# Kernel optimization log

Measured on AMD Instinct MI355X. Metric: run time of the kernel, lower is better.

The kernel has to match this reference:

```python
import jax, jax.numpy as jnp
import numpy as np

B, Qn, Kn, QD, KVD, FFN, H = 8, 1024, 2048, 512, 256, 2048, 8


def _layer_norm(x, g, b, eps=1e-5):
    m = jnp.mean(x, axis=-1, keepdims=True)
    v = jnp.mean((x - m) ** 2, axis=-1, keepdims=True)
    return (x - m) * jax.lax.rsqrt(v + eps) * g + b


def _mha(q, k, v, key_padding_mask, num_heads):
    # q,k: [B,S,D], v: [B,K,Dv]; reshape to per-head, scale by sqrt(key head dim)
    b, qn, d = q.shape
    kn = k.shape[1]
    dh = d // num_heads
    q = q.reshape(b, qn, num_heads, dh)
    k = k.reshape(b, kn, num_heads, dh)
    v = v.reshape(b, kn, num_heads, -1)
    attn = jnp.einsum('bqhd,bkhd->bhqk', q, k) / jnp.asarray(np.sqrt(dh), q.dtype)
    attn = jnp.where(key_padding_mask[:, None, None, :], -jnp.inf, attn)
    attn = jax.nn.softmax(attn, axis=-1)
    out = jnp.einsum('bhqk,bkhd->bqhd', attn, v)  # [B,Q,H,dv]
    return out.reshape(b, qn, -1)


def setup_inputs() -> dict:
    key = jax.random.key(0)
    ks = jax.random.split(key, 32)
    s = 0.02
    inp = {
        'queries_data': jax.random.normal(ks[0], (B, Qn, QD), jnp.float32),
        'queries_mask': jnp.zeros((B, Qn), bool),
        'box_pos': jax.random.normal(ks[1], (B, Qn, 4 * KVD), jnp.float32),
        'center_pos': jax.random.normal(ks[2], (B, Qn, 2 * KVD), jnp.float32),
        'kv_data': jax.random.normal(ks[3], (B, Kn, KVD), jnp.float32),
        'kv_mask': jnp.zeros((B, Kn), bool),
        'kv_pos': jax.random.normal(ks[4], (B, Kn, KVD), jnp.float32),
        # params ([in,out] convention)
        'sa_qkv_w': jax.random.normal(ks[5], (QD, 3 * QD), jnp.float32) * s,
        'sa_qkv_b': jnp.zeros((3 * QD,), jnp.float32),
        'sa_pos_w': jax.random.normal(ks[6], (4 * KVD, 2 * QD), jnp.float32) * s,
        'sa_pos_b': jnp.zeros((2 * QD,), jnp.float32),
        'sa_ln_g': jnp.ones((QD,), jnp.float32),
        'sa_ln_b': jnp.zeros((QD,), jnp.float32),
        'ca_q_w': jax.random.normal(ks[7], (QD, QD), jnp.float32) * s,
        'ca_q_b': jnp.zeros((QD,), jnp.float32),
        'ca_kv_w': jax.random.normal(ks[8], (KVD, 2 * QD), jnp.float32) * s,
        'ca_kv_b': jnp.zeros((2 * QD,), jnp.float32),
        'ca_qpos_w': jax.random.normal(ks[9], (2 * KVD, QD), jnp.float32) * s,
        'ca_qpos_b': jnp.zeros((QD,), jnp.float32),
        'ca_kpos_w': jax.random.normal(ks[10], (KVD, QD), jnp.float32) * s,
        'ca_kpos_b': jnp.zeros((QD,), jnp.float32),
        'ca_ln_g': jnp.ones((QD,), jnp.float32),
        'ca_ln_b': jnp.zeros((QD,), jnp.float32),
        'ffn_w1': jax.random.normal(ks[11], (QD, FFN), jnp.float32) * s,
        'ffn_b1': jnp.zeros((FFN,), jnp.float32),
        'ffn_w2': jax.random.normal(ks[12], (FFN, QD), jnp.float32) * s,
        'ffn_b2': jnp.zeros((QD,), jnp.float32),
        'ffn_ln_g': jnp.ones((QD,), jnp.float32),
        'ffn_ln_b': jnp.zeros((QD,), jnp.float32),
    }
    return inp


def reference(queries_data, queries_mask, box_pos, center_pos, kv_data, kv_mask, kv_pos,
              sa_qkv_w, sa_qkv_b, sa_pos_w, sa_pos_b, sa_ln_g, sa_ln_b,
              ca_q_w, ca_q_b, ca_kv_w, ca_kv_b, ca_qpos_w, ca_qpos_b,
              ca_kpos_w, ca_kpos_b, ca_ln_g, ca_ln_b,
              ffn_w1, ffn_b1, ffn_w2, ffn_b2, ffn_ln_g, ffn_ln_b):
    # ---- self-attention (pos added to q,k) ----
    qkv = queries_data @ sa_qkv_w + sa_qkv_b
    q, k, v = jnp.split(qkv, 3, axis=-1)
    q_pos, k_pos = jnp.split(box_pos @ sa_pos_w + sa_pos_b, 2, axis=-1)
    sa_out = _mha(q + q_pos, k + k_pos, v, queries_mask, H)
    sa_out = _layer_norm(queries_data + sa_out, sa_ln_g, sa_ln_b)
    # ---- cross-attention (pos concatenated per head) ----
    q = sa_out @ ca_q_w + ca_q_b
    k, v = jnp.split(kv_data @ ca_kv_w + ca_kv_b, 2, axis=-1)
    q_pos = center_pos @ ca_qpos_w + ca_qpos_b
    k_pos = kv_pos @ ca_kpos_w + ca_kpos_b
    dh = QD // H
    q = jnp.concatenate([q.reshape(B, Qn, H, dh), q_pos.reshape(B, Qn, H, dh)], axis=-1).reshape(B, Qn, -1)
    k = jnp.concatenate([k.reshape(B, Kn, H, dh), k_pos.reshape(B, Kn, H, dh)], axis=-1).reshape(B, Kn, -1)
    ca_out = _mha(q, k, v, kv_mask, H)
    ca_out = _layer_norm(sa_out + ca_out, ca_ln_g, ca_ln_b)
    # ---- FFN ----
    f = jax.nn.relu(ca_out @ ffn_w1 + ffn_b1) @ ffn_w2 + ffn_b2
    return _layer_norm(ca_out + f, ffn_ln_g, ffn_ln_b)
```

## Files before the change

kernel.cpp:

```cpp
#include <hip/hip_runtime.h>

typedef __attribute__((ext_vector_type(4))) float f32x4;
typedef __attribute__((ext_vector_type(8))) short bf16x8;
typedef __attribute__((ext_vector_type(4))) unsigned int u32x4;

static __device__ __forceinline__ float bf2f(short s){
    unsigned int u = ((unsigned int)(unsigned short)s) << 16;
    return __builtin_bit_cast(float, u);
}
static __device__ __forceinline__ short f2bf(float f){
    unsigned int u = __builtin_bit_cast(unsigned int, f);
    unsigned int r = (u + 0x7fffu + ((u >> 16) & 1u)) >> 16;
    return (short)r;
}
static __device__ __forceinline__ void gload_lds16(const void* g, void* l){
    __builtin_amdgcn_global_load_lds((const __attribute__((address_space(1))) void*)g,
                                     (__attribute__((address_space(3))) void*)l, 16, 0, 0);
}
static __device__ __forceinline__ float exp2fast(float x){
    float r; asm("v_exp_f32 %0, %1" : "=v"(r) : "v"(x)); return r;
}
static __device__ __forceinline__ unsigned int packbf(float lo, float hi){
#if __has_builtin(__builtin_amdgcn_perm)
    return __builtin_amdgcn_perm(__builtin_bit_cast(unsigned int, hi),
                                 __builtin_bit_cast(unsigned int, lo), 0x07060302u);
#else
    return (__builtin_bit_cast(unsigned int, hi) & 0xffff0000u) |
           (__builtin_bit_cast(unsigned int, lo) >> 16);
#endif
}
static __device__ __forceinline__ void prio_hi(){
#if defined(__HIP_DEVICE_COMPILE__)
    __builtin_amdgcn_s_setprio(1);
#endif
}
static __device__ __forceinline__ void prio_lo(){
#if defined(__HIP_DEVICE_COMPILE__)
    __builtin_amdgcn_s_setprio(0);
#endif
}

static __device__ __forceinline__ void transcast_body(const float* __restrict__ w,
                                                      short* __restrict__ wT,
                                                      int K, int N, int bx, int by, int t){
    int n = bx * 256 + t;
    int k0 = by * 8;
    bf16x8 o;
#pragma unroll
    for (int j = 0; j < 8; j++) o[j] = f2bf(w[(long)(k0 + j) * N + n]);
    *(bf16x8*)(wT + (long)n * K + k0) = o;
}
__global__ __launch_bounds__(256) void prep_weights(
    const float* __restrict__ queries, const float* __restrict__ box,
    const float* __restrict__ ctr, const float* __restrict__ kvd, const float* __restrict__ kvp,
    const unsigned char* __restrict__ qmask, const unsigned char* __restrict__ kmask,
    const float* __restrict__ b_qkv, const float* __restrict__ b_pos,
    short* __restrict__ Xcat, short* __restrict__ ctr_bf,
    short* __restrict__ kvd_bf, short* __restrict__ kvp_bf,
    float* __restrict__ mb_sa, float* __restrict__ mb_ca, float* __restrict__ bcomb,
    const float* __restrict__ w_qkv, const float* __restrict__ w_pos,
    const float* __restrict__ w_caq, const float* __restrict__ w_cakv,
    const float* __restrict__ w_caqp, const float* __restrict__ w_cakp,
    const float* __restrict__ w_f1, const float* __restrict__ w_f2,
    short* __restrict__ wTm_qk, short* __restrict__ wTv,
    short* __restrict__ wT_caq, short* __restrict__ wT_cakv,
    short* __restrict__ wT_caqp, short* __restrict__ wT_cakp,
    short* __restrict__ wT_f1, short* __restrict__ wT_f2)
{
    int bb = blockIdx.x, t = threadIdx.x;
    if (bb < 12288){
        const float* src; short* dst; long i; long stride; int logRow; int colOff;
        if (bb < 2048){ src = queries; dst = Xcat; i = ((long)bb * 256 + t) * 8; logRow = 9;  stride = 1536; colOff = 0; }
        else if (bb < 6144){ src = box; dst = Xcat; i = ((long)(bb - 2048) * 256 + t) * 8; logRow = 10; stride = 1536; colOff = 512; }
        else if (bb < 8192){ src = ctr; dst = ctr_bf; i = ((long)(bb - 6144) * 256 + t) * 8; logRow = 0; stride = 0; colOff = 0; }
        else if (bb < 10240){ src = kvd; dst = kvd_bf; i = ((long)(bb - 8192) * 256 + t) * 8; logRow = 0; stride = 0; colOff = 0; }
        else { src = kvp; dst = kvp_bf; i = ((long)(bb - 10240) * 256 + t) * 8; logRow = 0; stride = 0; colOff = 0; }
        f32x4 a = *(const f32x4*)(src + i);
        f32x4 b = *(const f32x4*)(src + i + 4);
        bf16x8 o;
#pragma unroll
        for (int j = 0; j < 4; j++){ o[j] = f2bf(a[j]); o[4 + j] = f2bf(b[j]); }
        long oi = logRow ? ((i >> logRow) * stride + colOff + (i & ((1L << logRow) - 1))) : i;
        *(bf16x8*)(dst + oi) = o;
        return;
    }
    if (bb < 12320){ int i = (bb - 12288) * 256 + t; mb_sa[i] = qmask[i] ? -1e30f : 0.f; return; }
    if (bb < 12384){ int i = (bb - 12320) * 256 + t; mb_ca[i] = kmask[i] ? -1e30f : 0.f; return; }
    if (bb < 12388){ int i = (bb - 12384) * 256 + t; if (i < 1024) bcomb[i] = b_qkv[i] + b_pos[i]; return; }
    int wb = bb - 12388;
    if (wb < 768){
        int by = wb / 4, bx = wb % 4;
        int n = bx * 256 + t;
        int k0 = by * 8;
        bf16x8 o;
#pragma unroll
        for (int j = 0; j < 8; j++){
            int kk = k0 + j;
            float v = (kk < 512) ? w_qkv[(long)kk * 1536 + n] : w_pos[(long)(kk - 512) * 1024 + n];
            o[j] = f2bf(v);
        }
        *(bf16x8*)(wTm_qk + (long)n * 1536 + k0) = o;
    }
    else if (wb < 896){
        int lb = wb - 768;
        int by = lb / 2, bx = lb % 2;
        int n = bx * 256 + t;
        int k0 = by * 8;
        bf16x8 o;
#pragma unroll
        for (int j = 0; j < 8; j++) o[j] = f2bf(w_qkv[(long)(k0 + j) * 1536 + 1024 + n]);
        *(bf16x8*)(wTv + (long)n * 512 + k0) = o;
    }
    else if (wb < 1024){ int lb = wb - 896;  transcast_body(w_caq,  wT_caq,  512, 512,  lb % 2, lb / 2, t); }
    else if (wb < 1152){ int lb = wb - 1024; transcast_body(w_cakv, wT_cakv, 256, 1024, lb % 4, lb / 4, t); }
    else if (wb < 1280){ int lb = wb - 1152; transcast_body(w_caqp, wT_caqp, 512, 512,  lb % 2, lb / 2, t); }
    else if (wb < 1344){ int lb = wb - 1280; transcast_body(w_cakp, wT_cakp, 256, 512,  lb % 2, lb / 2, t); }
    else if (wb < 1856){ int lb = wb - 1344; transcast_body(w_f1,   wT_f1,   512, 2048, lb % 8, lb / 8, t); }
    else               { int lb = wb - 1856; transcast_body(w_f2,   wT_f2,   2048, 512, lb % 2, lb / 2, t); }
}

struct GD {
    const short* A; const short* Bt; const float* bias;
    short* Cbf; float* Cf; short* Vt;
    long lda;
    int N, K, flags, vtColBase, snShift, vtSN, blkStart, nbx, nblk;
};
struct GD6 { GD g[6]; int n; };

static __device__ void gemm_body(char* smem, const GD6& dd, int bb)
{
    constexpr int BN = 128, BLOCK = 256;
    constexpr int BUF = (128 + BN) * 32;
    constexpr int EST = BN + 4;
    float* lC = (float*)smem;
    int si = 0;
#pragma unroll
    for (int i = 1; i < 6; i++) if (i < dd.n && bb >= dd.g[i].blkStart) si = i;
    const short* A = dd.g[si].A;
    const short* Bt = dd.g[si].Bt;
    const float* bias = dd.g[si].bias;
    short* Cbf = dd.g[si].Cbf;
    float* Cf = dd.g[si].Cf;
    short* Vt = dd.g[si].Vt;
    long lda = dd.g[si].lda;
    int N = dd.g[si].N, K = dd.g[si].K, flags = dd.g[si].flags;
    int vtColBase = dd.g[si].vtColBase, snShift = dd.g[si].snShift, vtSN = dd.g[si].vtSN;
    int nbx = dd.g[si].nbx, nblk = dd.g[si].nblk;

    int t = threadIdx.x, w = t >> 6, l = t & 63;
    int cl = l & 15, g = l >> 4;
    int flat = bb - dd.g[si].blkStart;
    int q8 = nblk >> 3;
    int swz = (flat & 7) * q8 + (flat >> 3);
    long r0 = (long)(swz / nbx) * 128, c0 = (long)(swz % nbx) * BN;
    int wr = w >> 1, wc = w & 1;
    f32x4 acc[4][4];
#pragma unroll
    for (int mi = 0; mi < 4; mi++)
#pragma unroll
        for (int ni = 0; ni < 4; ni++) acc[mi][ni] = f32x4{0.f, 0.f, 0.f, 0.f};

    auto stage = [&](int d, int k0){
        char* lA = smem + (size_t)d * BUF * 2;
        char* lB = lA + 128 * 32 * 2;
#pragma unroll
        for (int i = 0; i < 2; i++){
            int s = i * BLOCK + t;
            int row = s >> 2, blk = s & 3;
            int sb = blk ^ (row & 3);
            gload_lds16(A + (r0 + row) * lda + k0 + sb * 8, lA + i * 4096 + w * 1024);
        }
#pragma unroll
        for (int i = 0; i < 2; i++){
            int s = i * BLOCK + t;
            int row = s >> 2, blk = s & 3;
            int sb = blk ^ (row & 3);
            gload_lds16(Bt + (c0 + row) * (long)K + k0 + sb * 8, lB + i * 4096 + w * 1024);
        }
    };

    stage(0, 0);
    __syncthreads();
    int NK = K / 32;
    for (int kt = 0; kt < NK; kt++){
        int cur = kt & 1;
        if (kt + 1 < NK) stage(cur ^ 1, (kt + 1) * 32);
        const short* lA = (const short*)(smem + (size_t)cur * BUF * 2);
        const short* lB = lA + 128 * 32;
        bf16x8 af[4], bfr[4];
#pragma unroll
        for (int mi = 0; mi < 4; mi++){
            int row = wr * 64 + mi * 16 + cl;
            af[mi] = *(const bf16x8*)(lA + row * 32 + (g ^ (row & 3)) * 8);
        }
#pragma unroll
        for (int ni = 0; ni < 4; ni++){
            int row = wc * 64 + ni * 16 + cl;
            bfr[ni] = *(const bf16x8*)(lB + row * 32 + (g ^ (row & 3)) * 8);
        }
        prio_hi();
#pragma unroll
        for (int mi = 0; mi < 4; mi++)
#pragma unroll
            for (int ni = 0; ni < 4; ni++)
                acc[mi][ni] = __builtin_amdgcn_mfma_f32_16x16x32_bf16(af[mi], bfr[ni], acc[mi][ni], 0, 0, 0);
        prio_lo();
        __syncthreads();
    }

    bool vtBlock = (flags & 4) && (c0 >= vtColBase);
#pragma unroll
    for (int mi = 0; mi < 4; mi++){
        __syncthreads();
#pragma unroll
        for (int ni = 0; ni < 4; ni++)
#pragma unroll
            for (int rr = 0; rr < 4; rr++)
                lC[(wr * 16 + g * 4 + rr) * EST + wc * 64 + ni * 16 + cl] = acc[mi][ni][rr];
        __syncthreads();
        if (vtBlock){
#pragma unroll
            for (int c2 = 0; c2 < 2; c2++){
                int task = t + BLOCK * c2;
                int col = task & (BN - 1);
                int wrg = (task >> 7) & 1;
                int ch = task >> 8;
                float bv = bias[c0 + col];
                long qg0 = r0 + wrg * 64 + mi * 16 + ch * 8;
                bf16x8 ob;
#pragma unroll
                for (int j = 0; j < 8; j++)
                    ob[j] = f2bf(lC[(wrg * 16 + ch * 8 + j) * EST + col] + bv);
                long dvg = c0 - vtColBase + col;
                long h = dvg >> 6, dvv = dvg & 63;
                long b = qg0 >> snShift;
                long loc = qg0 & ((1L << snShift) - 1);
                *(bf16x8*)(Vt + ((b * 8 + h) * 64 + dvv) * (long)vtSN + loc) = ob;
            }
        } else {
            constexpr int CPR = BN / 8;
#pragma unroll
            for (int c2 = 0; c2 < 32 * CPR / BLOCK; c2++){
                int chunk = t + BLOCK * c2;
                int row = chunk / CPR;
                int coloff = (chunk % CPR) * 8;
                long grow = r0 + (row >> 4) * 64 + mi * 16 + (row & 15);
                long gcol = c0 + coloff;
                f32x4 bv0 = *(const f32x4*)(bias + gcol);
                f32x4 bv1 = *(const f32x4*)(bias + gcol + 4);
                float v[8];
#pragma unroll
                for (int j = 0; j < 8; j++){
                    float x = lC[row * EST + coloff + j] + (j < 4 ? bv0[j] : bv1[j - 4]);
                    if (flags & 1) x = fmaxf(x, 0.f);
                    v[j] = x;
                }
                if (Cf){
                    *(f32x4*)(Cf + grow * N + gcol) = f32x4{v[0], v[1], v[2], v[3]};
                    *(f32x4*)(Cf + grow * N + gcol + 4) = f32x4{v[4], v[5], v[6], v[7]};
                } else {
                    bf16x8 ob;
#pragma unroll
                    for (int j = 0; j < 8; j++) ob[j] = f2bf(v[j]);
                    long idx;
                    if (flags & 2){
                        long part = gcol >> 9;
                        long cc = gcol & 511;
                        long b = grow >> 10, qn = grow & 1023;
                        long h = cc >> 6, d = cc & 63;
                        idx = ((part * 64 + b * 8 + h) * 1024 + qn) * 64 + d;
                    } else if (flags & 4){
                        idx = grow * (long)vtColBase + gcol;
                    } else {
                        idx = grow * N + gcol;
                    }
                    *(bf16x8*)(Cbf + idx) = ob;
                }
            }
        }
    }
}

__global__ __launch_bounds__(256, 4) void gemm_multi(GD6 dd){
    __shared__ __attribute__((aligned(16))) char smem[32768];
    gemm_body(smem, dd, blockIdx.x);
}

struct AttnArgs {
    const short *Q1, *Q2, *K1, *K2, *Vt;
    const float* mbias; short* out; float scale2;
};

template<int DH, int KN, bool CAT>
static __device__ void attn_body(char* smemraw, const AttnArgs& a, int bid)
{
    constexpr int KT = 64, DV = 64, Qn = 1024, H = 8;
    constexpr int NF = DH / 32;
    constexpr int BPR = DH / 8;
    constexpr int KITER = KT * BPR / 256;
    constexpr int NT = KN / KT;
    short (*lK)[KT * DH] = (short(*)[KT * DH])smemraw;
    short (*lV)[DV * KT] = (short(*)[DV * KT])(smemraw + 2 * KT * DH * 2);
    const short* Q1 = a.Q1; const short* Q2 = a.Q2;
    const short* K1 = a.K1; const short* K2 = a.K2;
    const short* Vt = a.Vt;
    float scale2 = a.scale2;
    int t = threadIdx.x, w = t >> 6, l = t & 63;
    int cl = l & 15, g = l >> 4;
    int bh = (bid & 7) * 8 + (bid >> 6);
    int qb = (bid >> 3) & 7;
    int b = bh >> 3, h = bh & 7;
    int q0 = qb * 128 + w * 32;

    bf16x8 qf[2][NF];
#pragma unroll
    for (int qq = 0; qq < 2; qq++)
#pragma unroll
        for (int f = 0; f < NF; f++){
            if constexpr (CAT){
                const short* src = (f < NF / 2) ? Q1 : Q2;
                qf[qq][f] = *(const bf16x8*)(src + ((long)b * Qn + q0 + qq * 16 + cl) * 512 + h * 64
                                             + (f & (NF / 2 - 1)) * 32 + 8 * g);
            } else {
                qf[qq][f] = *(const bf16x8*)(Q1 + ((long)bh * Qn + q0 + qq * 16 + cl) * DH + f * 32 + 8 * g);
            }
        }

    const short* kp[KITER];
    long kstep[KITER];
#pragma unroll
    for (int i = 0; i < KITER; i++){
        int s_ = i * 256 + t;
        int srow_ = s_ / BPR, blk = s_ % BPR;
        int s32 = srow_ & 31;
        int key = (srow_ & 32) + 8 * ((s32 >> 2) & 3) + 4 * (s32 >> 4) + (s32 & 3);
        int sb = blk ^ (srow_ & 7);
        if constexpr (CAT){
            if (sb < 8){ kp[i] = K1 + ((long)b * KN + key) * 512 + h * 64 + sb * 8; kstep[i] = (long)KT * 512; }
            else       { kp[i] = K2 + ((long)b * KN + key) * 512 + h * 64 + (sb - 8) * 8; kstep[i] = (long)KT * 512; }
        } else {
            kp[i] = K1 + ((long)bh * KN + key) * DH + sb * 8; kstep[i] = (long)KT * DH;
        }
    }
    const short* vp[2];
#pragma unroll
    for (int i = 0; i < 2; i++){
        int s_ = i * 256 + t;
        int srow_ = s_ >> 3, blk = s_ & 7;
        int sb = blk ^ (srow_ & 7);
        vp[i] = Vt + ((long)bh * DV + srow_) * KN + sb * 8;
    }

    auto stage = [&](int d){
#pragma unroll
        for (int i = 0; i < KITER; i++){
            gload_lds16(kp[i], (char*)(&lK[d][0]) + i * 4096 + w * 1024);
            kp[i] += kstep[i];
        }
#pragma unroll
        for (int i = 0; i < 2; i++){
            gload_lds16(vp[i], (char*)(&lV[d][0]) + i * 4096 + w * 1024);
            vp[i] += KT;
        }
    };

    f32x4 st[2][4];
    auto do_qk = [&](int d){
        prio_hi();
#pragma unroll
        for (int o = 0; o < 4; o++){
            int srow_ = o * 16 + cl;
            bf16x8 kf[NF];
#pragma unroll
            for (int f = 0; f < NF; f++){
                int sb = (4 * f + g) ^ (srow_ & 7);
                kf[f] = *(const bf16x8*)(&lK[d][0] + srow_ * DH + sb * 8);
            }
#pragma unroll
            for (int qq = 0; qq < 2; qq++){
                f32x4 acc = f32x4{0.f, 0.f, 0.f, 0.f};
#pragma unroll
                for (int f = 0; f < NF; f++)
                    acc = __builtin_amdgcn_mfma_f32_16x16x32_bf16(kf[f], qf[qq][f], acc, 0, 0, 0);
                st[qq][o] = acc;
            }
        }
        prio_lo();
    };

    const float* mrow = a.mbias + (long)b * KN;
    bf16x8 vones;
    {
        u32x4 ou; ou[0] = ou[1] = ou[2] = ou[3] = 0x3F803F80u;
        vones = __builtin_bit_cast(bf16x8, ou);
    }
    f32x4 lacc[2];
    f32x4 oacc[2][4];
#pragma unroll
    for (int qq = 0; qq < 2; qq++){
        lacc[qq] = f32x4{0.f, 0.f, 0.f, 0.f};
#pragma unroll
        for (int d = 0; d < 4; d++) oacc[qq][d] = f32x4{0.f, 0.f, 0.f, 0.f};
    }

    f32x4 mb[4];
#pragma unroll
    for (int o = 0; o < 4; o++)
        mb[o] = *(const f32x4*)(mrow + (o >> 1) * 32 + 8 * g + 4 * (o & 1));

    stage(0);
    __syncthreads();
    do_qk(0);

    for (int tt = 0; tt < NT; tt++){
        int cur = tt & 1;
        if (tt + 1 < NT) stage(cur ^ 1);

        bf16x8 pa[2][2];
#pragma unroll
        for (int qq = 0; qq < 2; qq++){
#pragma unroll
            for (int kb = 0; kb < 2; kb++){
                float pA[4], pB[4];
#pragma unroll
                for (int rr = 0; rr < 4; rr++){
                    pA[rr] = exp2fast(fmaf(st[qq][2 * kb][rr], scale2, mb[2 * kb][rr]));
                    pB[rr] = exp2fast(fmaf(st[qq][2 * kb + 1][rr], scale2, mb[2 * kb + 1][rr]));
                }
                u32x4 pk;
                pk[0] = packbf(pA[0], pA[1]);
                pk[1] = packbf(pA[2], pA[3]);
                pk[2] = packbf(pB[0], pB[1]);
                pk[3] = packbf(pB[2], pB[3]);
                pa[qq][kb] = __builtin_bit_cast(bf16x8, pk);
            }
        }
        if (tt + 1 < NT){
#pragma unroll
            for (int o = 0; o < 4; o++)
                mb[o] = *(const f32x4*)(mrow + (tt + 1) * KT + (o >> 1) * 32 + 8 * g + 4 * (o & 1));
        }
        prio_hi();
#pragma unroll
        for (int qq = 0; qq < 2; qq++){
            lacc[qq] = __builtin_amdgcn_mfma_f32_16x16x32_bf16(pa[qq][0], vones, lacc[qq], 0, 0, 0);
            lacc[qq] = __builtin_amdgcn_mfma_f32_16x16x32_bf16(pa[qq][1], vones, lacc[qq], 0, 0, 0);
        }
#pragma unroll
        for (int dvc = 0; dvc < 4; dvc++){
            int vrow = dvc * 16 + cl;
            bf16x8 vf[2];
#pragma unroll
            for (int kb = 0; kb < 2; kb++){
                int sb = (4 * kb + g) ^ (vrow & 7);
                vf[kb] = *(const bf16x8*)(&lV[cur][0] + vrow * KT + sb * 8);
            }
#pragma unroll
            for (int qq = 0; qq < 2; qq++){
                f32x4 o = oacc[qq][dvc];
                o = __builtin_amdgcn_mfma_f32_16x16x32_bf16(pa[qq][0], vf[0], o, 0, 0, 0);
                o = __builtin_amdgcn_mfma_f32_16x16x32_bf16(pa[qq][1], vf[1], o, 0, 0, 0);
                oacc[qq][dvc] = o;
            }
        }
        prio_lo();
        __syncthreads();
        if (tt + 1 < NT) do_qk(cur ^ 1);
    }

#pragma unroll
    for (int qq = 0; qq < 2; qq++){
        float linv[4];
#pragma unroll
        for (int rr = 0; rr < 4; rr++) linv[rr] = 1.f / lacc[qq][rr];
#pragma unroll
        for (int dvc = 0; dvc < 4; dvc++)
#pragma unroll
            for (int rr = 0; rr < 4; rr++){
                int q = q0 + qq * 16 + 4 * g + rr;
                a.out[(((long)b * Qn + q) * H + h) * DV + dvc * 16 + cl] = f2bf(oacc[qq][dvc][rr] * linv[rr]);
            }
    }
}

__global__ __launch_bounds__(256, 2) void attn_ca(AttnArgs a){
    __shared__ __attribute__((aligned(16))) char smem[2 * 64 * 128 * 2 + 2 * 64 * 64 * 2];
    attn_body<128, 2048, true>(smem, a, blockIdx.x);
}

__global__ __launch_bounds__(256, 2) void attn_sa_gemm(AttnArgs a, GD6 dd, int nAttn){
    __shared__ __attribute__((aligned(16))) char smem[32768];
    if ((int)blockIdx.x < nAttn) attn_body<64, 1024, false>(smem, a, blockIdx.x);
    else gemm_body(smem, dd, blockIdx.x - nAttn);
}

__global__ __launch_bounds__(256) void ln_fuse(const float* __restrict__ a, const short* __restrict__ b,
                                               const float* __restrict__ g, const float* __restrict__ be,
                                               float* __restrict__ outf, short* __restrict__ outb){
    int w = threadIdx.x >> 6, l = threadIdx.x & 63;
    long row = (long)blockIdx.x * 4 + w;
    long base = row * 512 + l * 8;
    f32x4 a0 = *(const f32x4*)(a + base);
    f32x4 a1 = *(const f32x4*)(a + base + 4);
    bf16x8 bb = *(const bf16x8*)(b + base);
    float x[8]; float s = 0.f, s2 = 0.f;
#pragma unroll
    for (int j = 0; j < 4; j++){ x[j] = a0[j] + bf2f(bb[j]); x[4 + j] = a1[j] + bf2f(bb[4 + j]); }
#pragma unroll
    for (int j = 0; j < 8; j++){ s += x[j]; s2 += x[j] * x[j]; }
#pragma unroll
    for (int o = 1; o < 64; o <<= 1){ s += __shfl_xor(s, o); s2 += __shfl_xor(s2, o); }
    float mean = s * (1.f / 512.f);
    float rstd = rsqrtf(s2 * (1.f / 512.f) - mean * mean + 1e-5f);
    int c = l * 8;
    f32x4 y0, y1; bf16x8 ob;
#pragma unroll
    for (int j = 0; j < 4; j++){
        float y = (x[j] - mean) * rstd * g[c + j] + be[c + j];
        y0[j] = y; ob[j] = f2bf(y);
    }
#pragma unroll
    for (int j = 0; j < 4; j++){
        float y = (x[4 + j] - mean) * rstd * g[c + 4 + j] + be[c + 4 + j];
        y1[j] = y; ob[4 + j] = f2bf(y);
    }
    *(f32x4*)(outf + base) = y0;
    *(f32x4*)(outf + base + 4) = y1;
    if (outb) *(bf16x8*)(outb + base) = ob;
}

extern "C" void kernel_launch(void* const* d_in, const int* in_sizes, int n_in,
                              void* d_out, int out_size, void* d_ws, size_t ws_size,
                              hipStream_t stream)
{
    (void)in_sizes; (void)n_in; (void)out_size; (void)ws_size;
    const int Qn = 1024, Kn = 2048;
    const long MQ = 8L * Qn;
    const long MK = 8L * Kn;

    const float* queries = (const float*)d_in[0];
    const unsigned char* qmask = (const unsigned char*)d_in[1];
    const float* box  = (const float*)d_in[2];
    const float* ctr  = (const float*)d_in[3];
    const float* kvd  = (const float*)d_in[4];
    const unsigned char* kmask = (const unsigned char*)d_in[5];
    const float* kvp  = (const float*)d_in[6];
    const float* w_qkv = (const float*)d_in[7];  const float* b_qkv = (const float*)d_in[8];
    const float* w_pos = (const float*)d_in[9];  const float* b_pos = (const float*)d_in[10];
    const float* g_sa  = (const float*)d_in[11]; const float* be_sa = (const float*)d_in[12];
    const float* w_caq = (const float*)d_in[13]; const float* b_caq = (const float*)d_in[14];
    const float* w_cakv = (const float*)d_in[15]; const float* b_cakv = (const float*)d_in[16];
    const float* w_caqp = (const float*)d_in[17]; const float* b_caqp = (const float*)d_in[18];
    const float* w_cakp = (const float*)d_in[19]; const float* b_cakp = (const float*)d_in[20];
    const float* g_ca  = (const float*)d_in[21]; const float* be_ca = (const float*)d_in[22];
    const float* w_f1  = (const float*)d_in[23]; const float* b_f1 = (const float*)d_in[24];
    const float* w_f2  = (const float*)d_in[25]; const float* b_f2 = (const float*)d_in[26];
    const float* g_f   = (const float*)d_in[27]; const float* be_f = (const float*)d_in[28];

    char* ws = (char*)d_ws;
    size_t off = 0;
    auto alloc = [&](size_t bytes) -> char* {
        char* p = ws + off;
        off += (bytes + 255) & ~(size_t)255;
        return p;
    };
    short* wTm_qk  = (short*)alloc(1024L * 1536 * 2);
    short* wTv     = (short*)alloc(512L * 512 * 2);
    short* wT_caq  = (short*)alloc(512L * 512 * 2);
    short* wT_cakv = (short*)alloc(1024L * 256 * 2);
    short* wT_caqp = (short*)alloc(512L * 512 * 2);
    short* wT_cakp = (short*)alloc(512L * 256 * 2);
    short* wT_f1   = (short*)alloc(2048L * 512 * 2);
    short* wT_f2   = (short*)alloc(512L * 2048 * 2);
    float* bcomb   = (float*)alloc(1024L * 4);
    short* ctr_bf  = (short*)alloc(MQ * 512 * 2);
    short* kvd_bf  = (short*)alloc(MK * 256 * 2);
    short* kvp_bf  = (short*)alloc(MK * 256 * 2);
    short* saln_bf = (short*)alloc(MQ * 512 * 2);
    short* caln_bf = (short*)alloc(MQ * 512 * 2);
    float* sa_ln_f = (float*)alloc(MQ * 512 * 4);
    float* ca_ln_f = (float*)alloc(MQ * 512 * 4);
    short* att_bf  = (short*)alloc(MQ * 512 * 2);
    short* f_out   = (short*)alloc(MQ * 512 * 2);
    short* VtSA    = (short*)alloc(64L * 64 * 1024 * 2);
    short* VtCA    = (short*)alloc(64L * 64 * 2048 * 2);
    float* mb_sa   = (float*)alloc(MQ * 4);
    float* mb_ca   = (float*)alloc(MK * 4);
    short* caK     = (short*)alloc(MK * 512 * 2);
    short* cakp_bf = (short*)alloc(MK * 512 * 2);
    short* caq_bf  = (short*)alloc(MQ * 512 * 2);
    short* caqp_bf = (short*)alloc(MQ * 512 * 2);
    char* zone1 = alloc(MQ * 1536 * 2);
    char* zone2 = alloc(MQ * 2048 * 2);

    auto mkgd = [&](const short* A, long lda, const short* Bt, const float* bias,
                    short* Cbf, float* Cf, int M, int N, int K, int flags,
                    short* Vt, int vtColBase, int snShift, int vtSN, int blkStart) -> GD {
        GD d;
        d.A = A; d.Bt = Bt; d.bias = bias; d.Cbf = Cbf; d.Cf = Cf; d.Vt = Vt;
        d.lda = lda; d.N = N; d.K = K; d.flags = flags;
        d.vtColBase = vtColBase; d.snShift = snShift; d.vtSN = vtSN;
        d.blkStart = blkStart; d.nbx = N / 128; d.nblk = (N / 128) * (M / 128);
        return d;
    };
    auto pad_gd = [&](GD6& dd){
        for (int i = dd.n; i < 6; i++){ dd.g[i] = dd.g[0]; dd.g[i].blkStart = 0x7fffffff; }
    };
    auto launch_multi = [&](GD6& dd){
        int total = 0;
        for (int i = 0; i < dd.n; i++) total += dd.g[i].nblk;
        pad_gd(dd);
        gemm_multi<<<dim3(total), dim3(256), 0, stream>>>(dd);
    };

    short* Xcat = (short*)zone1;
    prep_weights<<<dim3(14756), dim3(256), 0, stream>>>(
        queries, box, ctr, kvd, kvp, qmask, kmask, b_qkv, b_pos,
        Xcat, ctr_bf, kvd_bf, kvp_bf, mb_sa, mb_ca, bcomb,
        w_qkv, w_pos, w_caq, w_cakv, w_caqp, w_cakp, w_f1, w_f2,
        wTm_qk, wTv, wT_caq, wT_cakv, wT_caqp, wT_cakp, wT_f1, wT_f2);

    short* QKVa = (short*)zone2;
    short* Qa  = QKVa;
    short* Ka  = QKVa + 64L * 1024 * 64;
    {
        GD6 dd; dd.n = 2;
        dd.g[0] = mkgd(Xcat, 1536, wTm_qk, bcomb, QKVa, nullptr, (int)MQ, 1024, 1536, 2,
                       nullptr, 0, 0, 0, 0);
        dd.g[1] = mkgd(Xcat, 1536, wTv, b_qkv + 1024, nullptr, nullptr, (int)MQ, 512, 512, 4,
                       VtSA, 0, 10, 1024, dd.g[0].nblk);
        launch_multi(dd);
    }

    {
        AttnArgs aa;
        aa.Q1 = Qa; aa.Q2 = nullptr; aa.K1 = Ka; aa.K2 = nullptr; aa.Vt = VtSA;
        aa.mbias = mb_sa; aa.out = att_bf; aa.scale2 = 0.125f * 1.44269504f;
        GD6 dd; dd.n = 3;
        int s0 = 0;
        dd.g[0] = mkgd(kvd_bf, 256, wT_cakv, b_cakv, caK, nullptr, (int)MK, 1024, 256, 4,
                       VtCA, 512, 11, 2048, s0);                    s0 += dd.g[0].nblk;
        dd.g[1] = mkgd(kvp_bf, 256, wT_cakp, b_cakp, cakp_bf, nullptr, (int)MK, 512, 256, 0,
                       nullptr, 0, 0, 0, s0);                       s0 += dd.g[1].nblk;
        dd.g[2] = mkgd(ctr_bf, 512, wT_caqp, b_caqp, caqp_bf, nullptr, (int)MQ, 512, 512, 0,
                       nullptr, 0, 0, 0, s0);                       s0 += dd.g[2].nblk;
        pad_gd(dd);
        attn_sa_gemm<<<dim3(512 + s0), dim3(256), 0, stream>>>(aa, dd, 512);
    }

    ln_fuse<<<dim3((unsigned)(MQ / 4)), dim3(256), 0, stream>>>(queries, att_bf, g_sa, be_sa, sa_ln_f, saln_bf);

    {
        GD6 dd; dd.n = 1;
        dd.g[0] = mkgd(saln_bf, 512, wT_caq, b_caq, caq_bf, nullptr, (int)MQ, 512, 512, 0,
                       nullptr, 0, 0, 0, 0);
        launch_multi(dd);
    }

    {
        AttnArgs aa;
        aa.Q1 = caq_bf; aa.Q2 = caqp_bf; aa.K1 = caK; aa.K2 = cakp_bf; aa.Vt = VtCA;
        aa.mbias = mb_ca; aa.out = att_bf; aa.scale2 = 0.08838834764831845f * 1.44269504f;
        attn_ca<<<dim3(512), dim3(256), 0, stream>>>(aa);
    }

    ln_fuse<<<dim3((unsigned)(MQ / 4)), dim3(256), 0, stream>>>(sa_ln_f, att_bf, g_ca, be_ca, ca_ln_f, caln_bf);

    short* mid_bf = (short*)zone2;
    {
        GD6 dd; dd.n = 1;
        dd.g[0] = mkgd(caln_bf, 512, wT_f1, b_f1, mid_bf, nullptr, (int)MQ, 2048, 512, 1,
                       nullptr, 0, 0, 0, 0);
        launch_multi(dd);
    }
    {
        GD6 dd; dd.n = 1;
        dd.g[0] = mkgd(mid_bf, 2048, wT_f2, b_f2, f_out, nullptr, (int)MQ, 512, 2048, 0,
                       nullptr, 0, 0, 0, 0);
        launch_multi(dd);
    }

    ln_fuse<<<dim3((unsigned)(MQ / 4)), dim3(256), 0, stream>>>(ca_ln_f, f_out, g_f, be_f, (float*)d_out, (short*)nullptr);
}
```

Before: 292.5 us.

## Split attention key range in two and merge partials in layer norm

Both attention kernels now split the key dimension into two halves, launching twice as many blocks (1024 instead of 512). Each block writes an unnormalised bf16 output and its row sums to per-part buffers. A new ln_fuse_split kernel adds the two partial outputs, divides by the summed denominators, and applies the residual and layer norm. The aim is better CU occupancy on a 512-block grid. In exchange the kernels write more intermediate output traffic, and the partial numerators are rounded to bf16 before normalisation, with no running-max rescaling, since the softmax here has no max subtraction.

Result: slower. 298.9 us (+2.2%).

```diff
diff --git a/kernel.cpp b/kernel.cpp
--- a/kernel.cpp
+++ b/kernel.cpp
@@ -288,17 +288,17 @@
 
 struct AttnArgs {
     const short *Q1, *Q2, *K1, *K2, *Vt;
-    const float* mbias; short* out; float scale2;
+    const float* mbias; short* out; float* outL; float scale2;
 };
 
 template<int DH, int KN, bool CAT>
-static __device__ void attn_body(char* smemraw, const AttnArgs& a, int bid)
+static __device__ void attn_body(char* smemraw, const AttnArgs& a, int bid, int part,
+                                 int key0base, int nt)
 {
     constexpr int KT = 64, DV = 64, Qn = 1024, H = 8;
     constexpr int NF = DH / 32;
     constexpr int BPR = DH / 8;
     constexpr int KITER = KT * BPR / 256;
-    constexpr int NT = KN / KT;
     short (*lK)[KT * DH] = (short(*)[KT * DH])smemraw;
     short (*lV)[DV * KT] = (short(*)[DV * KT])(smemraw + 2 * KT * DH * 2);
     const short* Q1 = a.Q1; const short* Q2 = a.Q2;
@@ -336,10 +336,10 @@
         int key = (srow_ & 32) + 8 * ((s32 >> 2) & 3) + 4 * (s32 >> 4) + (s32 & 3);
         int sb = blk ^ (srow_ & 7);
         if constexpr (CAT){
-            if (sb < 8){ kp[i] = K1 + ((long)b * KN + key) * 512 + h * 64 + sb * 8; kstep[i] = (long)KT * 512; }
-            else       { kp[i] = K2 + ((long)b * KN + key) * 512 + h * 64 + (sb - 8) * 8; kstep[i] = (long)KT * 512; }
+            if (sb < 8){ kp[i] = K1 + ((long)(b * KN + key0base + key)) * 512 + h * 64 + sb * 8; kstep[i] = (long)KT * 512; }
+            else       { kp[i] = K2 + ((long)(b * KN + key0base + key)) * 512 + h * 64 + (sb - 8) * 8; kstep[i] = (long)KT * 512; }
         } else {
-            kp[i] = K1 + ((long)bh * KN + key) * DH + sb * 8; kstep[i] = (long)KT * DH;
+            kp[i] = K1 + ((long)bh * KN + key0base + key) * DH + sb * 8; kstep[i] = (long)KT * DH;
         }
     }
     const short* vp[2];
@@ -348,7 +348,7 @@
         int s_ = i * 256 + t;
         int srow_ = s_ >> 3, blk = s_ & 7;
         int sb = blk ^ (srow_ & 7);
-        vp[i] = Vt + ((long)bh * DV + srow_) * KN + sb * 8;
+        vp[i] = Vt + ((long)bh * DV + srow_) * KN + key0base + sb * 8;
     }
 
     auto stage = [&](int d){
@@ -388,7 +388,7 @@
         prio_lo();
     };
 
-    const float* mrow = a.mbias + (long)b * KN;
+    const float* mrow = a.mbias + (long)b * KN + key0base;
     bf16x8 vones;
     {
         u32x4 ou; ou[0] = ou[1] = ou[2] = ou[3] = 0x3F803F80u;
@@ -412,9 +412,9 @@
     __syncthreads();
     do_qk(0);
 
-    for (int tt = 0; tt < NT; tt++){
+    for (int tt = 0; tt < nt; tt++){
         int cur = tt & 1;
-        if (tt + 1 < NT) stage(cur ^ 1);
+        if (tt + 1 < nt) stage(cur ^ 1);
 
         bf16x8 pa[2][2];
 #pragma unroll
@@ -435,7 +435,7 @@
                 pa[qq][kb] = __builtin_bit_cast(bf16x8, pk);
             }
         }
-        if (tt + 1 < NT){
+        if (tt + 1 < nt){
 #pragma unroll
             for (int o = 0; o < 4; o++)
                 mb[o] = *(const f32x4*)(mrow + (tt + 1) * KT + (o >> 1) * 32 + 8 * g + 4 * (o & 1));
@@ -465,33 +465,89 @@
         }
         prio_lo();
         __syncthreads();
-        if (tt + 1 < NT) do_qk(cur ^ 1);
-    }
-
+        if (tt + 1 < nt) do_qk(cur ^ 1);
+    }
+
+    long obase = (long)part * 8192 * 512;
 #pragma unroll
     for (int qq = 0; qq < 2; qq++){
-        float linv[4];
-#pragma unroll
-        for (int rr = 0; rr < 4; rr++) linv[rr] = 1.f / lacc[qq][rr];
-#pragma unroll
-        for (int dvc = 0; dvc < 4; dvc++)
+        if (cl == 0){
 #pragma unroll
             for (int rr = 0; rr < 4; rr++){
                 int q = q0 + qq * 16 + 4 * g + rr;
-                a.out[(((long)b * Qn + q) * H + h) * DV + dvc * 16 + cl] = f2bf(oacc[qq][dvc][rr] * linv[rr]);
+                a.outL[(long)part * 65536 + (long)bh * 1024 + q] = lacc[qq][rr];
+            }
+        }
+#pragma unroll
+        for (int dvc = 0; dvc < 4; dvc++)
+#pragma unroll
+            for (int rr = 0; rr < 4; rr++){
+                int q = q0 + qq * 16 + 4 * g + rr;
+                a.out[obase + (((long)b * Qn + q) * H + h) * DV + dvc * 16 + cl] = f2bf(oacc[qq][dvc][rr]);
             }
     }
 }
 
 __global__ __launch_bounds__(256, 2) void attn_ca(AttnArgs a){
     __shared__ __attribute__((aligned(16))) char smem[2 * 64 * 128 * 2 + 2 * 64 * 64 * 2];
-    attn_body<128, 2048, true>(smem, a, blockIdx.x);
+    int part = blockIdx.x >> 9;
+    attn_body<128, 2048, true>(smem, a, blockIdx.x & 511, part, part * 1024, 16);
 }
 
 __global__ __launch_bounds__(256, 2) void attn_sa_gemm(AttnArgs a, GD6 dd, int nAttn){
     __shared__ __attribute__((aligned(16))) char smem[32768];
-    if ((int)blockIdx.x < nAttn) attn_body<64, 1024, false>(smem, a, blockIdx.x);
-    else gemm_body(smem, dd, blockIdx.x - nAttn);
+    if ((int)blockIdx.x < nAttn){
+        int part = blockIdx.x >> 9;
+        attn_body<64, 1024, false>(smem, a, blockIdx.x & 511, part, part * 512, 8);
+    } else {
+        gemm_body(smem, dd, blockIdx.x - nAttn);
+    }
+}
+
+__global__ __launch_bounds__(256) void ln_fuse_split(
+    const float* __restrict__ a, const short* __restrict__ O, const float* __restrict__ L,
+    const float* __restrict__ g, const float* __restrict__ be,
+    float* __restrict__ outf, short* __restrict__ outb)
+{
+    int w = threadIdx.x >> 6, l = threadIdx.x & 63;
+    long row = (long)blockIdx.x * 4 + w;
+    long base = row * 512 + l * 8;
+    long b = row >> 10, q = row & 1023;
+    int h = l >> 3;
+    float l0 = L[(b * 8 + h) * 1024 + q];
+    float l1 = L[65536 + (b * 8 + h) * 1024 + q];
+    float linv = 1.f / (l0 + l1);
+    f32x4 a0 = *(const f32x4*)(a + base);
+    f32x4 a1 = *(const f32x4*)(a + base + 4);
+    bf16x8 o0 = *(const bf16x8*)(O + base);
+    bf16x8 o1 = *(const bf16x8*)(O + 8192L * 512 + base);
+    float x[8]; float s = 0.f, s2 = 0.f;
+#pragma unroll
+    for (int j = 0; j < 4; j++){
+        x[j] = a0[j] + (bf2f(o0[j]) + bf2f(o1[j])) * linv;
+        x[4 + j] = a1[j] + (bf2f(o0[4 + j]) + bf2f(o1[4 + j])) * linv;
+    }
+#pragma unroll
+    for (int j = 0; j < 8; j++){ s += x[j]; s2 += x[j] * x[j]; }
+#pragma unroll
+    for (int o = 1; o < 64; o <<= 1){ s += __shfl_xor(s, o); s2 += __shfl_xor(s2, o); }
+    float mean = s * (1.f / 512.f);
+    float rstd = rsqrtf(s2 * (1.f / 512.f) - mean * mean + 1e-5f);
+    int c = l * 8;
+    f32x4 y0, y1; bf16x8 ob;
+#pragma unroll
+    for (int j = 0; j < 4; j++){
+        float y = (x[j] - mean) * rstd * g[c + j] + be[c + j];
+        y0[j] = y; ob[j] = f2bf(y);
+    }
+#pragma unroll
+    for (int j = 0; j < 4; j++){
+        float y = (x[4 + j] - mean) * rstd * g[c + 4 + j] + be[c + 4 + j];
+        y1[j] = y; ob[4 + j] = f2bf(y);
+    }
+    *(f32x4*)(outf + base) = y0;
+    *(f32x4*)(outf + base + 4) = y1;
+    if (outb) *(bf16x8*)(outb + base) = ob;
 }
 
 __global__ __launch_bounds__(256) void ln_fuse(const float* __restrict__ a, const short* __restrict__ b,
@@ -580,7 +636,8 @@
     short* caln_bf = (short*)alloc(MQ * 512 * 2);
     float* sa_ln_f = (float*)alloc(MQ * 512 * 4);
     float* ca_ln_f = (float*)alloc(MQ * 512 * 4);
-    short* att_bf  = (short*)alloc(MQ * 512 * 2);
+    short* attO    = (short*)alloc(2L * MQ * 512 * 2);
+    float* attL    = (float*)alloc(2L * 65536 * 4);
     short* f_out   = (short*)alloc(MQ * 512 * 2);
     short* VtSA    = (short*)alloc(64L * 64 * 1024 * 2);
     short* VtCA    = (short*)alloc(64L * 64 * 2048 * 2);
@@ -635,7 +692,7 @@
     {
         AttnArgs aa;
         aa.Q1 = Qa; aa.Q2 = nullptr; aa.K1 = Ka; aa.K2 = nullptr; aa.Vt = VtSA;
-        aa.mbias = mb_sa; aa.out = att_bf; aa.scale2 = 0.125f * 1.44269504f;
+        aa.mbias = mb_sa; aa.out = attO; aa.outL = attL; aa.scale2 = 0.125f * 1.44269504f;
         GD6 dd; dd.n = 3;
         int s0 = 0;
         dd.g[0] = mkgd(kvd_bf, 256, wT_cakv, b_cakv, caK, nullptr, (int)MK, 1024, 256, 4,
@@ -645,10 +702,11 @@
         dd.g[2] = mkgd(ctr_bf, 512, wT_caqp, b_caqp, caqp_bf, nullptr, (int)MQ, 512, 512, 0,
                        nullptr, 0, 0, 0, s0);                       s0 += dd.g[2].nblk;
         pad_gd(dd);
-        attn_sa_gemm<<<dim3(512 + s0), dim3(256), 0, stream>>>(aa, dd, 512);
-    }
-
-    ln_fuse<<<dim3((unsigned)(MQ / 4)), dim3(256), 0, stream>>>(queries, att_bf, g_sa, be_sa, sa_ln_f, saln_bf);
+        attn_sa_gemm<<<dim3(1024 + s0), dim3(256), 0, stream>>>(aa, dd, 1024);
+    }
+
+    ln_fuse_split<<<dim3((unsigned)(MQ / 4)), dim3(256), 0, stream>>>(
+        queries, attO, attL, g_sa, be_sa, sa_ln_f, saln_bf);
 
     {
         GD6 dd; dd.n = 1;
@@ -660,11 +718,12 @@
     {
         AttnArgs aa;
         aa.Q1 = caq_bf; aa.Q2 = caqp_bf; aa.K1 = caK; aa.K2 = cakp_bf; aa.Vt = VtCA;
-        aa.mbias = mb_ca; aa.out = att_bf; aa.scale2 = 0.08838834764831845f * 1.44269504f;
-        attn_ca<<<dim3(512), dim3(256), 0, stream>>>(aa);
-    }
-
-    ln_fuse<<<dim3((unsigned)(MQ / 4)), dim3(256), 0, stream>>>(sa_ln_f, att_bf, g_ca, be_ca, ca_ln_f, caln_bf);
+        aa.mbias = mb_ca; aa.out = attO; aa.outL = attL; aa.scale2 = 0.08838834764831845f * 1.44269504f;
+        attn_ca<<<dim3(1024), dim3(256), 0, stream>>>(aa);
+    }
+
+    ln_fuse_split<<<dim3((unsigned)(MQ / 4)), dim3(256), 0, stream>>>(
+        sa_ln_f, attO, attL, g_ca, be_ca, ca_ln_f, caln_bf);
 
     short* mid_bf = (short*)zone2;
     {
```
